# Kernel tuning notes

Hardware: AMD Instinct MI355X
Metric: run time of the kernel (lower is better)

## Reference

```python
import jax, jax.numpy as jnp
import numpy as np

N = 100000      # nodes
E = 1600000     # edges (avg degree 16)
F = 128         # nfeats
H = 4           # nheads
D = 16          # nhid // nheads
ALPHA = 0.2     # LeakyReLU negative slope


def setup_inputs() -> dict:
    key = jax.random.key(0)
    k0, k1, k2, k3, k4 = jax.random.split(key, 5)
    h = jax.random.normal(k0, (N, F), dtype=jnp.float32)
    src = jax.random.randint(k1, (E,), 0, N)
    dst = jax.random.randint(k2, (E,), 0, N)
    # per-head Linear W (xavier_uniform gain=1.414 approx) and attention vector a
    limW = 1.414 * np.sqrt(6.0 / (F + D))
    W = jax.random.uniform(k3, (H, F, D), jnp.float32, -limW, limW)
    Wb = jnp.zeros((H, D), jnp.float32)
    lima = 1.414 * np.sqrt(6.0 / (2 * D + 1))
    a = jax.random.uniform(k4, (H, 2 * D), jnp.float32, -lima, lima)
    ab = jnp.zeros((H,), jnp.float32)
    return {"h": h, "W": W, "Wb": Wb, "a": a, "ab": ab, "src": src, "dst": dst}


def reference(h, W, Wb, a, ab, src, dst):
    # Per-head linear projection (dropout is identity in eval mode)
    Wh = jnp.einsum('nf,hfd->nhd', h, W) + Wb          # [N,H,D]
    Whs = Wh[src]                                       # [E,H,D] gather src
    Whd = Wh[dst]                                       # [E,H,D] gather dst
    # e = leakyrelu(a . [Wh_src || Wh_dst])
    e = (jnp.einsum('ehd,hd->eh', Whs, a[:, :D]) +
         jnp.einsum('ehd,hd->eh', Whd, a[:, D:]) + ab)  # [E,H]
    e = jnp.where(e > 0, e, ALPHA * e)
    # segment softmax over incoming edges per dst node
    m = jax.ops.segment_max(e, dst, num_segments=N)     # [N,H]
    m = jnp.where(jnp.isfinite(m), m, 0.0)
    p = jnp.exp(e - m[dst])                             # [E,H]
    denom = jax.ops.segment_sum(p, dst, num_segments=N) # [N,H]
    num = jax.ops.segment_sum(p[:, :, None] * Whs, dst, num_segments=N)  # [N,H,D]
    h_prime = num / jnp.maximum(denom, 1e-9)[:, :, None]
    # concat heads -> [N, H*D]; rows of nodes with no in-edges are zero
    return h_prime.reshape(N, H * D)
```

## Files before the change

### kernel.cpp

```cpp
#include <hip/hip_runtime.h>
#include <hip/hip_bf16.h>
#include <math.h>

#define N_NODES 100000
#define N_EDGES 1600000
#define NF 128
#define NH 4
#define ND 16
#define GAT_ALPHA 0.2f

#define BSHIFT 8
#define NBK 391
#define CAPB 5120
#define CAPH 2816
#define EPB 8192
#define EBLK 196
#define PBLK 391
#define NTILES ((N_NODES + 63) / 64)

typedef __attribute__((ext_vector_type(8))) __bf16 bf16x8;
typedef __attribute__((ext_vector_type(4))) float f32x4;

#define PADK 136

__global__ __launch_bounds__(256) void k_prep(
    const float* __restrict__ W, const float* __restrict__ a,
    int* __restrict__ gcur, __hip_bfloat16* __restrict__ Btg)
{
    const int hh = blockIdx.x;
    const int t = threadIdx.x;

    if (hh == 0)
        for (int i = t; i < 512; i += 256) gcur[i] = 0;

    for (int idx = t; idx < 2048; idx += 256) {
        int d = idx & 15, f = idx >> 4;
        Btg[(hh * 16 + d) * 128 + f] =
            __float2bfloat16(W[hh * (NF * ND) + f * ND + d]);
    }
    for (int idx = t; idx < 256; idx += 256) {
        int f = idx & 127, which = idx >> 7;
        float s = 0.f;
        #pragma unroll
        for (int d = 0; d < 16; d++)
            s = fmaf(W[hh * (NF * ND) + f * ND + d], a[hh * 32 + which * 16 + d], s);
        Btg[(64 + which * 8 + hh) * 128 + f] = __float2bfloat16(s);
    }
    for (int idx = t; idx < 256; idx += 256) {
        int f = idx & 127, which = idx >> 7;
        Btg[(68 + which * 8 + hh) * 128 + f] = __float2bfloat16(0.f);
    }
}

__global__ __launch_bounds__(256) void k_fused(
    const float* __restrict__ h, const __hip_bfloat16* __restrict__ Btg,
    const float* __restrict__ Wb, const float* __restrict__ a,
    const float* __restrict__ ab, const int* __restrict__ src,
    const int* __restrict__ dst, int* __restrict__ gcur,
    uint* __restrict__ sb, __hip_bfloat16* __restrict__ Whb,
    float* __restrict__ es, float* __restrict__ ed)
{
    __shared__ __align__(16) __hip_bfloat16 Bt[80 * PADK];
    __shared__ int hist[NBK];
    __shared__ int cur[NBK];

    const int tid = threadIdx.x;

    if (blockIdx.x < EBLK) {
        const int base = blockIdx.x * EPB;
        const int lim = min(EPB, N_EDGES - base);

        for (int i = tid; i < NBK; i += 256) hist[i] = 0;
        __syncthreads();
        for (int i = tid; i < lim; i += 256)
            atomicAdd(&hist[dst[base + i] >> BSHIFT], 1);
        __syncthreads();
        for (int i = tid; i < NBK; i += 256) {
            int v = hist[i];
            cur[i] = v ? atomicAdd(&gcur[i], v) : 0;
        }
        __syncthreads();
        for (int i = tid; i < lim; i += 256) {
            int d = dst[base + i];
            int bk = d >> BSHIFT;
            int pos = atomicAdd(&cur[bk], 1);
            if (pos < CAPB)
                sb[bk * CAPB + pos] = (uint)(src[base + i] | ((d & 255) << 17));
        }
        return;
    }

    const int pb = blockIdx.x - EBLK;
    const int wv = tid >> 6;
    const int l = tid & 63;
    const int m = l & 15;
    const int quad = l >> 4;

    for (int c = tid; c < 80 * 128 / 8; c += 256) {
        int row = c >> 4, col = (c & 15) * 8;
        *(float4*)&Bt[row * PADK + col] = ((const float4*)Btg)[c];
    }

    float wb4[4];
    #pragma unroll
    for (int t = 0; t < 4; t++) wb4[t] = Wb[t * 16 + m];
    float eb = 0.f;
    if (m < 4) {
        #pragma unroll
        for (int d = 0; d < 16; d++) eb = fmaf(Wb[m * 16 + d], a[m * 32 + d], eb);
    } else if (m >= 8 && m < 12) {
        int hh = m - 8;
        #pragma unroll
        for (int d = 0; d < 16; d++)
            eb = fmaf(Wb[hh * 16 + d], a[hh * 32 + 16 + d], eb);
        eb += ab[hh];
    }
    __syncthreads();

    for (int tile = pb; tile < NTILES; tile += PBLK) {
        const int node = tile * 64 + wv * 16 + m;
        const bool ok = node < N_NODES;
        const float4* hrow = (const float4*)(h + (size_t)(ok ? node : 0) * NF);

        f32x4 acc[5];
        #pragma unroll
        for (int t = 0; t < 5; t++) acc[t] = (f32x4){0.f, 0.f, 0.f, 0.f};

        #pragma unroll
        for (int kk = 0; kk < 4; kk++) {
            bf16x8 af;
            if (ok) {
                float4 v0 = hrow[kk * 8 + quad * 2];
                float4 v1 = hrow[kk * 8 + quad * 2 + 1];
                af[0] = (__bf16)v0.x; af[1] = (__bf16)v0.y;
                af[2] = (__bf16)v0.z; af[3] = (__bf16)v0.w;
                af[4] = (__bf16)v1.x; af[5] = (__bf16)v1.y;
                af[6] = (__bf16)v1.z; af[7] = (__bf16)v1.w;
            } else {
                #pragma unroll
                for (int j = 0; j < 8; j++) af[j] = (__bf16)0.f;
            }
            #pragma unroll
            for (int t = 0; t < 5; t++) {
                bf16x8 bf = *(const bf16x8*)&Bt[(t * 16 + m) * PADK + kk * 32 + quad * 8];
                acc[t] = __builtin_amdgcn_mfma_f32_16x16x32_bf16(af, bf, acc[t], 0, 0, 0);
            }
        }

        const int nodeb = tile * 64 + wv * 16 + quad * 4;
        #pragma unroll
        for (int r = 0; r < 4; r++) {
            int n = nodeb + r;
            if (n < N_NODES) {
                #pragma unroll
                for (int t = 0; t < 4; t++)
                    Whb[n * 64 + t * 16 + m] = __float2bfloat16(acc[t][r] + wb4[t]);
                float ev = acc[4][r] + eb;
                if (m < 4) es[n * 4 + m] = ev;
                else if (m >= 8 && m < 12) ed[n * 4 + (m - 8)] = ev;
            }
        }
    }
}

__global__ __launch_bounds__(512) void k_bucket(
    const uint* __restrict__ sb, const int* __restrict__ gcur,
    const __hip_bfloat16* __restrict__ Whb, const float* __restrict__ es,
    const float* __restrict__ ed, float* __restrict__ out)
{
    __shared__ int ssl[CAPH];
    __shared__ int ncnt[128];
    __shared__ int noff[128];
    __shared__ int ncur[128];
    __shared__ int wsum[2];
    __shared__ float pu_all[8][256];

    const int b  = blockIdx.x >> 1;
    const int hf = blockIdx.x & 1;
    const int t  = threadIdx.x;
    const int l  = t & 63;
    const int wid = t >> 6;

    const int ebase = b * CAPB;
    const int ecnt = min(gcur[b], CAPB);
    const int dlo = hf << 7;

    if (t < 128) ncnt[t] = 0;
    __syncthreads();

    for (int i = t; i < ecnt; i += 512) {
        int dn = (int)(sb[ebase + i] >> 17) - dlo;
        if ((unsigned)dn < 128u) atomicAdd(&ncnt[dn], 1);
    }
    __syncthreads();

    {
        int v = (t < 128) ? ncnt[t] : 0;
        int x = v;
        #pragma unroll
        for (int o = 1; o < 64; o <<= 1) {
            int y = __shfl_up(x, o);
            if (l >= o) x += y;
        }
        if (l == 63 && wid < 2) wsum[wid] = x;
        __syncthreads();
        if (t < 128) {
            int add = (wid == 1) ? wsum[0] : 0;
            int excl = x + add - v;
            noff[t] = excl;
            ncur[t] = excl;
        }
    }
    __syncthreads();

    for (int i = t; i < ecnt; i += 512) {
        uint v = sb[ebase + i];
        int dn = (int)(v >> 17) - dlo;
        if ((unsigned)dn < 128u) {
            int pos = atomicAdd(&ncur[dn], 1);
            if (pos < CAPH) ssl[pos] = (int)(v & 0x1FFFFu);
        }
    }
    __syncthreads();

    const int r = l & 15;
    const int q = l >> 4;
    const int hh = r >> 2;
    const float4* es4 = (const float4*)es;
    const uint2* Wu2 = (const uint2*)Whb;
    float* pu = &pu_all[wid][0];
    const float* pu_q = pu + q * 4 + hh;

    for (int k = 0; k < 16; k++) {
        const int ln = wid * 16 + k;
        const int node = b * 256 + dlo + ln;
        if (node >= N_NODES) break;

        int start = noff[ln];
        int deg = ncnt[ln];
        if (start >= CAPH) deg = 0;
        else deg = min(deg, CAPH - start);

        const float4 edv = ((const float4*)ed)[node];

        float acc0 = 0.f, acc1 = 0.f, acc2 = 0.f, acc3 = 0.f, den = 0.f;

        for (int bst = 0; bst < deg; bst += 64) {
            int nchunk = min(64, deg - bst);

            float4 p4 = make_float4(0.f, 0.f, 0.f, 0.f);
            if (l < nchunk) {
                int sl = ssl[start + bst + l];
                float4 esv = es4[sl];
                float x;
                x = esv.x + edv.x; p4.x = __expf(fmaxf(x, GAT_ALPHA * x));
                x = esv.y + edv.y; p4.y = __expf(fmaxf(x, GAT_ALPHA * x));
                x = esv.z + edv.z; p4.z = __expf(fmaxf(x, GAT_ALPHA * x));
                x = esv.w + edv.w; p4.w = __expf(fmaxf(x, GAT_ALPHA * x));
            }
            ((float4*)pu)[l] = p4;

            const int last = start + deg - 1;
            #pragma unroll 4
            for (int jj = 0; jj < nchunk; jj += 4) {
                int ee = min(start + bst + jj + q, last);
                int s = ssl[ee];
                float p = pu_q[jj * 4];
                uint2 v = Wu2[s * 16 + r];
                acc0 = fmaf(p, __uint_as_float(v.x << 16), acc0);
                acc1 = fmaf(p, __uint_as_float(v.x & 0xffff0000u), acc1);
                acc2 = fmaf(p, __uint_as_float(v.y << 16), acc2);
                acc3 = fmaf(p, __uint_as_float(v.y & 0xffff0000u), acc3);
                den += p;
            }
        }

        acc0 += __shfl_xor(acc0, 16); acc1 += __shfl_xor(acc1, 16);
        acc2 += __shfl_xor(acc2, 16); acc3 += __shfl_xor(acc3, 16);
        den  += __shfl_xor(den, 16);
        acc0 += __shfl_xor(acc0, 32); acc1 += __shfl_xor(acc1, 32);
        acc2 += __shfl_xor(acc2, 32); acc3 += __shfl_xor(acc3, 32);
        den  += __shfl_xor(den, 32);

        if (q == 0) {
            float rr = 1.0f / fmaxf(den, 1e-9f);
            ((float4*)out)[node * 16 + r] =
                make_float4(acc0 * rr, acc1 * rr, acc2 * rr, acc3 * rr);
        }
    }
}

extern "C" void kernel_launch(void* const* d_in, const int* in_sizes, int n_in,
                              void* d_out, int out_size, void* d_ws, size_t ws_size,
                              hipStream_t stream)
{
    const float* h  = (const float*)d_in[0];
    const float* W  = (const float*)d_in[1];
    const float* Wb = (const float*)d_in[2];
    const float* a  = (const float*)d_in[3];
    const float* ab = (const float*)d_in[4];
    const int* src  = (const int*)d_in[5];
    const int* dst  = (const int*)d_in[6];
    float* out = (float*)d_out;

    char* w = (char*)d_ws;
    __hip_bfloat16* Whb = (__hip_bfloat16*)w; w += (size_t)N_NODES * 64 * 2;
    float* es      = (float*)w;  w += (size_t)N_NODES * 4 * 4;
    float* ed      = (float*)w;  w += (size_t)N_NODES * 4 * 4;
    uint* sb       = (uint*)w;   w += (size_t)NBK * CAPB * 4;
    int* gcur      = (int*)w;    w += 512 * 4;
    __hip_bfloat16* Btg = (__hip_bfloat16*)w; w += 80 * 128 * 2;

    k_prep<<<4, 256, 0, stream>>>(W, a, gcur, Btg);
    k_fused<<<EBLK + PBLK, 256, 0, stream>>>(h, Btg, Wb, a, ab, src, dst,
                                             gcur, sb, Whb, es, ed);
    k_bucket<<<NBK * 2, 512, 0, stream>>>(sb, gcur, Whb, es, ed, out);
}
```

Before: 198.1 us.

## Shrink dst buckets to 64 nodes and give each bucket one 256-thread block

The destination-bucket size drops from 256 to 64 nodes, giving 1563 buckets of capacity 1280. Each bucket is now handled by a single 256-thread block instead of two 512-thread half-bucket blocks. Previously each half-block scanned the whole bucket's edge list and discarded the other half, so this removes redundant global reads and filtering and simplifies the prefix scan to a single wavefront. To make room for the larger per-block histogram, the binning kernel aliases its shared histogram arrays onto the Bt tile buffer. The cost is more global atomics on gcur and a tighter per-bucket capacity, which raises the risk of overflow on skewed degree distributions.

```diff
diff --git a/kernel.cpp b/kernel.cpp
--- a/kernel.cpp
+++ b/kernel.cpp
@@ -9,10 +9,9 @@
 #define ND 16
 #define GAT_ALPHA 0.2f
 
-#define BSHIFT 8
-#define NBK 391
-#define CAPB 5120
-#define CAPH 2816
+#define BSHIFT 6
+#define NBK 1563
+#define CAPB 1280
 #define EPB 8192
 #define EBLK 196
 #define PBLK 391
@@ -31,7 +30,7 @@
     const int t = threadIdx.x;
 
     if (hh == 0)
-        for (int i = t; i < 512; i += 256) gcur[i] = 0;
+        for (int i = t; i < 2048; i += 256) gcur[i] = 0;
 
     for (int idx = t; idx < 2048; idx += 256) {
         int d = idx & 15, f = idx >> 4;
@@ -60,13 +59,13 @@
     uint* __restrict__ sb, __hip_bfloat16* __restrict__ Whb,
     float* __restrict__ es, float* __restrict__ ed)
 {
-    __shared__ __align__(16) __hip_bfloat16 Bt[80 * PADK];
-    __shared__ int hist[NBK];
-    __shared__ int cur[NBK];
+    __shared__ __align__(16) char smem[80 * PADK * 2];
 
     const int tid = threadIdx.x;
 
     if (blockIdx.x < EBLK) {
+        int* hist = (int*)smem;
+        int* cur  = hist + NBK;
         const int base = blockIdx.x * EPB;
         const int lim = min(EPB, N_EDGES - base);
 
@@ -85,11 +84,12 @@
             int bk = d >> BSHIFT;
             int pos = atomicAdd(&cur[bk], 1);
             if (pos < CAPB)
-                sb[bk * CAPB + pos] = (uint)(src[base + i] | ((d & 255) << 17));
+                sb[bk * CAPB + pos] = (uint)(src[base + i] | ((d & 63) << 17));
         }
         return;
     }
 
+    __hip_bfloat16* Bt = (__hip_bfloat16*)smem;
     const int pb = blockIdx.x - EBLK;
     const int wv = tid >> 6;
     const int l = tid & 63;
@@ -163,63 +163,50 @@
     }
 }
 
-__global__ __launch_bounds__(512) void k_bucket(
+__global__ __launch_bounds__(256) void k_bucket(
     const uint* __restrict__ sb, const int* __restrict__ gcur,
     const __hip_bfloat16* __restrict__ Whb, const float* __restrict__ es,
     const float* __restrict__ ed, float* __restrict__ out)
 {
-    __shared__ int ssl[CAPH];
-    __shared__ int ncnt[128];
-    __shared__ int noff[128];
-    __shared__ int ncur[128];
-    __shared__ int wsum[2];
-    __shared__ float pu_all[8][256];
-
-    const int b  = blockIdx.x >> 1;
-    const int hf = blockIdx.x & 1;
+    __shared__ int ssl[CAPB];
+    __shared__ int ncnt[64];
+    __shared__ int noff[64];
+    __shared__ int ncur[64];
+    __shared__ float pu_all[4][256];
+
+    const int b  = blockIdx.x;
     const int t  = threadIdx.x;
     const int l  = t & 63;
     const int wid = t >> 6;
 
     const int ebase = b * CAPB;
     const int ecnt = min(gcur[b], CAPB);
-    const int dlo = hf << 7;
-
-    if (t < 128) ncnt[t] = 0;
-    __syncthreads();
-
-    for (int i = t; i < ecnt; i += 512) {
-        int dn = (int)(sb[ebase + i] >> 17) - dlo;
-        if ((unsigned)dn < 128u) atomicAdd(&ncnt[dn], 1);
-    }
-    __syncthreads();
-
-    {
-        int v = (t < 128) ? ncnt[t] : 0;
+
+    if (t < 64) ncnt[t] = 0;
+    __syncthreads();
+
+    for (int i = t; i < ecnt; i += 256)
+        atomicAdd(&ncnt[(sb[ebase + i] >> 17) & 63], 1);
+    __syncthreads();
+
+    if (t < 64) {
+        int v = ncnt[t];
         int x = v;
         #pragma unroll
         for (int o = 1; o < 64; o <<= 1) {
             int y = __shfl_up(x, o);
             if (l >= o) x += y;
         }
-        if (l == 63 && wid < 2) wsum[wid] = x;
-        __syncthreads();
-        if (t < 128) {
-            int add = (wid == 1) ? wsum[0] : 0;
-            int excl = x + add - v;
-            noff[t] = excl;
-            ncur[t] = excl;
-        }
-    }
-    __syncthreads();
-
-    for (int i = t; i < ecnt; i += 512) {
+        noff[t] = x - v;
+        ncur[t] = x - v;
+    }
+    __syncthreads();
+
+    for (int i = t; i < ecnt; i += 256) {
         uint v = sb[ebase + i];
-        int dn = (int)(v >> 17) - dlo;
-        if ((unsigned)dn < 128u) {
-            int pos = atomicAdd(&ncur[dn], 1);
-            if (pos < CAPH) ssl[pos] = (int)(v & 0x1FFFFu);
-        }
+        int dn = (int)(v >> 17) & 63;
+        int pos = atomicAdd(&ncur[dn], 1);
+        if (pos < CAPB) ssl[pos] = (int)(v & 0x1FFFFu);
     }
     __syncthreads();
 
@@ -233,13 +220,13 @@
 
     for (int k = 0; k < 16; k++) {
         const int ln = wid * 16 + k;
-        const int node = b * 256 + dlo + ln;
+        const int node = b * 64 + ln;
         if (node >= N_NODES) break;
 
         int start = noff[ln];
         int deg = ncnt[ln];
-        if (start >= CAPH) deg = 0;
-        else deg = min(deg, CAPH - start);
+        if (start >= CAPB) deg = 0;
+        else deg = min(deg, CAPB - start);
 
         const float4 edv = ((const float4*)ed)[node];
 
@@ -308,11 +295,11 @@
     float* es      = (float*)w;  w += (size_t)N_NODES * 4 * 4;
     float* ed      = (float*)w;  w += (size_t)N_NODES * 4 * 4;
     uint* sb       = (uint*)w;   w += (size_t)NBK * CAPB * 4;
-    int* gcur      = (int*)w;    w += 512 * 4;
+    int* gcur      = (int*)w;    w += 2048 * 4;
     __hip_bfloat16* Btg = (__hip_bfloat16*)w; w += 80 * 128 * 2;
 
     k_prep<<<4, 256, 0, stream>>>(W, a, gcur, Btg);
     k_fused<<<EBLK + PBLK, 256, 0, stream>>>(h, Btg, Wb, a, ab, src, dst,
                                              gcur, sb, Whb, es, ed);
-    k_bucket<<<NBK * 2, 512, 0, stream>>>(sb, gcur, Whb, es, ed, out);
+    k_bucket<<<NBK, 256, 0, stream>>>(sb, gcur, Whb, es, ed, out);
 }
```

New measurement: 205.2 us. +3.6%, slower.
